# Performance work log

Measured on AMD Instinct MI355X. Metric: run time of the kernel, lower is better.

Reference implementation:

```python
import jax, jax.numpy as jnp
import numpy as np

# ---- module hyperparams (match init_kwargs) ----
REGIONS_DIMS = [0, 1, 2, 4, 9, 16]
ALL_DIM = sum(REGIONS_DIMS)          # 32
NUM_REGIONS = len(REGIONS_DIMS)      # 6
FIELD_NUM = 32
VOCAB = 200000
BATCH = 8192
TEMPERATURE = 1.0
EPS = 1e-5                            # torch BatchNorm1d default eps


def _build_region_mask():
    """Replicates init_variables(): row 0 is all-zero (drop-feature region),
    rows 1..R-1 are disjoint consecutive segments of sizes REGIONS_DIMS[1:]."""
    mask = np.zeros((NUM_REGIONS, ALL_DIM), dtype=np.float32)
    dims_pre_sum = [0] + [sum(REGIONS_DIMS[1:i]) for i in range(2, NUM_REGIONS)]
    for r, (pre, dim) in enumerate(zip(dims_pre_sum, REGIONS_DIMS[1:]), start=1):
        mask[r, pre:pre + dim] = 1.0
    return jnp.asarray(mask)


def setup_inputs() -> dict:
    key = jax.random.key(0)
    k_ids, k_emb, k_w = jax.random.split(key, 3)
    input_ids = jax.random.randint(k_ids, (BATCH, FIELD_NUM), 0, VOCAB, dtype=jnp.int64)
    # torch.nn.init.uniform_(a=-0.05, b=0.05)
    emb_table = jax.random.uniform(k_emb, (VOCAB, ALL_DIM), dtype=jnp.float32,
                                   minval=-0.05, maxval=0.05)
    # xavier_uniform on [F, R, 1]: bound = sqrt(6/(R+1))
    bound = float(np.sqrt(6.0 / (NUM_REGIONS + 1)))
    field_region_weights = jax.random.uniform(
        k_w, (FIELD_NUM, NUM_REGIONS, 1), dtype=jnp.float32, minval=-bound, maxval=bound)
    return {
        "input_ids": input_ids,
        "emb_table": emb_table,
        "field_region_weights": field_region_weights,
        "region_mask": _build_region_mask(),
    }


def reference(input_ids, emb_table, field_region_weights, region_mask):
    # Embedding gather: [B, F, D]
    emb = emb_table[input_ids]
    # BatchNorm1d(field_num, affine=False), training mode: per-field stats over (batch, D),
    # biased variance (torch normalizes with biased var).
    mean = jnp.mean(emb, axis=(0, 2), keepdims=True)
    var = jnp.var(emb, axis=(0, 2), keepdims=True)
    x = (emb - mean) * jax.lax.rsqrt(var + EPS)
    # softmax over regions: [F, R]
    w = jax.nn.softmax(field_region_weights[..., 0] / TEMPERATURE, axis=1)
    # sum_r w[f,r] * mask[r,d] -> per-(field, dim) scale; equivalent to the original's
    # broadcast-to-[B,F,R,D], multiply, and sum over R, without the big intermediate.
    coef = jnp.einsum('fr,rd->fd', w, region_mask)
    return x * coef[None, :, :]
```

## Files before the change

### kernel.cpp

```cpp
#include <hip/hip_runtime.h>
#include <math.h>

#define BATCH    8192
#define FIELDS   32
#define DIM      32
#define NREG     6
#define EPS      1e-5f
#define NBLKA    4096
#define PBASE    64


__global__ __launch_bounds__(256) void irazor_stats_kernel(
        const int*   __restrict__ ids,
        const float* __restrict__ table,
        float*       __restrict__ ws) {
    const int t   = threadIdx.x;
    const int blk = blockIdx.x;
    const int f   = t >> 3;
    const int vec = t & 7;

    float s = 0.f, sq = 0.f;
    #pragma unroll
    for (int i = 0; i < 2; ++i) {
        const int id = ids[(blk * 2 + i) * FIELDS + f];
        const float4 v = *reinterpret_cast<const float4*>(
            table + (size_t)id * DIM + vec * 4);
        s  += v.x + v.y + v.z + v.w;
        sq += v.x * v.x + v.y * v.y + v.z * v.z + v.w * v.w;
    }

    #pragma unroll
    for (int off = 1; off < 8; off <<= 1) {
        s  += __shfl_xor(s, off);
        sq += __shfl_xor(sq, off);
    }
    if (vec == 0) {
        ws[PBASE + f * NBLKA + blk]        = s;
        ws[PBASE + (32 + f) * NBLKA + blk] = sq;
    }
}

__global__ __launch_bounds__(256) void irazor_reduce_kernel(float* __restrict__ ws) {
    const int slot = blockIdx.x;
    const int t    = threadIdx.x;
    const float* __restrict__ p = ws + PBASE + (size_t)slot * NBLKA;
    float acc = 0.f;
    #pragma unroll
    for (int i = 0; i < NBLKA / 256; ++i) acc += p[i * 256 + t];
    #pragma unroll
    for (int off = 1; off < 64; off <<= 1) acc += __shfl_xor(acc, off);
    __shared__ float l[4];
    if ((t & 63) == 0) l[t >> 6] = acc;
    __syncthreads();
    if (t == 0) ws[slot] = l[0] + l[1] + l[2] + l[3];
}

__global__ __launch_bounds__(256) void irazor_out_kernel(
        const int*   __restrict__ ids,
        const float* __restrict__ table,
        const float* __restrict__ frw,
        const float* __restrict__ mask,
        const float* __restrict__ ws,
        float*       __restrict__ out) {
    const int t   = threadIdx.x;
    const int blk = blockIdx.x;

    __shared__ float scoef[FIELDS][DIM];
    {
        const int f2 = t & 31;
        const int q  = t >> 5;
        float w[NREG]; float m = -1e30f;
        #pragma unroll
        for (int r = 0; r < NREG; ++r) { w[r] = frw[f2 * NREG + r]; m = fmaxf(m, w[r]); }
        float ssum = 0.f;
        #pragma unroll
        for (int r = 0; r < NREG; ++r) { w[r] = __expf(w[r] - m); ssum += w[r]; }
        const float inv = 1.f / ssum;
        #pragma unroll
        for (int dd = 0; dd < 4; ++dd) {
            const int d = q * 4 + dd;
            float c = 0.f;
            #pragma unroll
            for (int r = 0; r < NREG; ++r) c += w[r] * mask[r * DIM + d];
            scoef[f2][d] = c * inv;
        }
    }
    __syncthreads();

    const int f   = t >> 3;
    const int vec = t & 7;
    const float invN = 1.f / (float)(BATCH * DIM);
    const float mean = ws[f] * invN;
    const float var  = ws[32 + f] * invN - mean * mean;
    const float istd = rsqrtf(var + EPS);
    const float4 c = *reinterpret_cast<const float4*>(&scoef[f][vec * 4]);

    float4* __restrict__ out4 = reinterpret_cast<float4*>(out);
    #pragma unroll
    for (int i = 0; i < 2; ++i) {
        const int id = ids[(blk * 2 + i) * FIELDS + f];
        const float4 v = *reinterpret_cast<const float4*>(
            table + (size_t)id * DIM + vec * 4);
        float4 o;
        o.x = (v.x - mean) * istd * c.x;
        o.y = (v.y - mean) * istd * c.y;
        o.z = (v.z - mean) * istd * c.z;
        o.w = (v.w - mean) * istd * c.w;
        out4[(size_t)blk * 512 + (size_t)i * 256 + t] = o;
    }
}

extern "C" void kernel_launch(void* const* d_in, const int* in_sizes, int n_in,
                              void* d_out, int out_size, void* d_ws, size_t ws_size,
                              hipStream_t stream) {
    const int*   ids   = (const int*)d_in[0];
    const float* table = (const float*)d_in[1];
    const float* frw   = (const float*)d_in[2];
    const float* mask  = (const float*)d_in[3];
    float*       out   = (float*)d_out;
    float*       ws    = (float*)d_ws;

    irazor_stats_kernel<<<NBLKA, 256, 0, stream>>>(ids, table, ws);
    irazor_reduce_kernel<<<64, 256, 0, stream>>>(ws);
    irazor_out_kernel<<<NBLKA, 256, 0, stream>>>(ids, table, frw, mask, ws, out);
}
```

Baseline: 100.1 us.

## Stage gathered embeddings in output buffer and apply precomputed scale/bias in place

The stats kernel now writes each gathered embedding row into the output buffer while accumulating sums. A finalize kernel reduces the partial sums per field and folds mean, inverse std and softmax region coefficients into per-(field,dim) scale and bias. The apply kernel then rewrites the output in place with one FMA, instead of re-gathering random table rows. This replaces a second random gather with a sequential read plus an extra full-size write.

```diff
diff --git a/kernel.cpp b/kernel.cpp
--- a/kernel.cpp
+++ b/kernel.cpp
@@ -8,23 +8,28 @@
 #define EPS      1e-5f
 #define NBLKA    4096
 #define PBASE    64
+#define SCALE_F  (PBASE + 64 * NBLKA)
+#define BIAS_F   (SCALE_F + FIELDS * DIM)
 
 
-__global__ __launch_bounds__(256) void irazor_stats_kernel(
+__global__ __launch_bounds__(256) void irazor_stage_stats_kernel(
         const int*   __restrict__ ids,
         const float* __restrict__ table,
-        float*       __restrict__ ws) {
+        float*       __restrict__ ws,
+        float*       __restrict__ out) {
     const int t   = threadIdx.x;
     const int blk = blockIdx.x;
     const int f   = t >> 3;
     const int vec = t & 7;
 
+    float4* __restrict__ out4 = reinterpret_cast<float4*>(out);
     float s = 0.f, sq = 0.f;
     #pragma unroll
     for (int i = 0; i < 2; ++i) {
         const int id = ids[(blk * 2 + i) * FIELDS + f];
         const float4 v = *reinterpret_cast<const float4*>(
             table + (size_t)id * DIM + vec * 4);
+        out4[(size_t)blk * 512 + (size_t)i * 256 + t] = v;
         s  += v.x + v.y + v.z + v.w;
         sq += v.x * v.x + v.y * v.y + v.z * v.z + v.w * v.w;
     }
@@ -40,73 +45,78 @@
     }
 }
 
-__global__ __launch_bounds__(256) void irazor_reduce_kernel(float* __restrict__ ws) {
-    const int slot = blockIdx.x;
-    const int t    = threadIdx.x;
-    const float* __restrict__ p = ws + PBASE + (size_t)slot * NBLKA;
-    float acc = 0.f;
+__global__ __launch_bounds__(256) void irazor_finalize_kernel(
+        const float* __restrict__ frw,
+        const float* __restrict__ mask,
+        float*       __restrict__ ws) {
+    const int fld = blockIdx.x;
+    const int t   = threadIdx.x;
+
+    const float* __restrict__ ps = ws + PBASE + (size_t)fld * NBLKA;
+    const float* __restrict__ pq = ws + PBASE + (size_t)(32 + fld) * NBLKA;
+    float a = 0.f, b = 0.f;
     #pragma unroll
-    for (int i = 0; i < NBLKA / 256; ++i) acc += p[i * 256 + t];
+    for (int i = 0; i < NBLKA / 256; ++i) {
+        a += ps[i * 256 + t];
+        b += pq[i * 256 + t];
+    }
     #pragma unroll
-    for (int off = 1; off < 64; off <<= 1) acc += __shfl_xor(acc, off);
-    __shared__ float l[4];
-    if ((t & 63) == 0) l[t >> 6] = acc;
+    for (int off = 1; off < 64; off <<= 1) {
+        a += __shfl_xor(a, off);
+        b += __shfl_xor(b, off);
+    }
+    __shared__ float ls[4], lq[4];
+    const int wave = t >> 6;
+    if ((t & 63) == 0) { ls[wave] = a; lq[wave] = b; }
     __syncthreads();
-    if (t == 0) ws[slot] = l[0] + l[1] + l[2] + l[3];
+    const float S  = ls[0] + ls[1] + ls[2] + ls[3];
+    const float SQ = lq[0] + lq[1] + lq[2] + lq[3];
+
+    if (t < DIM) {
+        const float invN = 1.f / (float)(BATCH * DIM);
+        const float mean = S * invN;
+        const float var  = SQ * invN - mean * mean;
+        const float istd = rsqrtf(var + EPS);
+
+        float w[NREG]; float m = -1e30f;
+        #pragma unroll
+        for (int r = 0; r < NREG; ++r) { w[r] = frw[fld * NREG + r]; m = fmaxf(m, w[r]); }
+        float ssum = 0.f;
+        #pragma unroll
+        for (int r = 0; r < NREG; ++r) { w[r] = __expf(w[r] - m); ssum += w[r]; }
+        float c = 0.f;
+        #pragma unroll
+        for (int r = 0; r < NREG; ++r) c += w[r] * mask[r * DIM + t];
+        c /= ssum;
+
+        const float sc = istd * c;
+        ws[SCALE_F + fld * DIM + t] = sc;
+        ws[BIAS_F  + fld * DIM + t] = -mean * sc;
+    }
 }
 
-__global__ __launch_bounds__(256) void irazor_out_kernel(
-        const int*   __restrict__ ids,
-        const float* __restrict__ table,
-        const float* __restrict__ frw,
-        const float* __restrict__ mask,
+__global__ __launch_bounds__(256) void irazor_apply_kernel(
         const float* __restrict__ ws,
         float*       __restrict__ out) {
     const int t   = threadIdx.x;
     const int blk = blockIdx.x;
-
-    __shared__ float scoef[FIELDS][DIM];
-    {
-        const int f2 = t & 31;
-        const int q  = t >> 5;
-        float w[NREG]; float m = -1e30f;
-        #pragma unroll
-        for (int r = 0; r < NREG; ++r) { w[r] = frw[f2 * NREG + r]; m = fmaxf(m, w[r]); }
-        float ssum = 0.f;
-        #pragma unroll
-        for (int r = 0; r < NREG; ++r) { w[r] = __expf(w[r] - m); ssum += w[r]; }
-        const float inv = 1.f / ssum;
-        #pragma unroll
-        for (int dd = 0; dd < 4; ++dd) {
-            const int d = q * 4 + dd;
-            float c = 0.f;
-            #pragma unroll
-            for (int r = 0; r < NREG; ++r) c += w[r] * mask[r * DIM + d];
-            scoef[f2][d] = c * inv;
-        }
-    }
-    __syncthreads();
-
     const int f   = t >> 3;
     const int vec = t & 7;
-    const float invN = 1.f / (float)(BATCH * DIM);
-    const float mean = ws[f] * invN;
-    const float var  = ws[32 + f] * invN - mean * mean;
-    const float istd = rsqrtf(var + EPS);
-    const float4 c = *reinterpret_cast<const float4*>(&scoef[f][vec * 4]);
+
+    const float4 sc = *reinterpret_cast<const float4*>(ws + SCALE_F + f * DIM + vec * 4);
+    const float4 bi = *reinterpret_cast<const float4*>(ws + BIAS_F  + f * DIM + vec * 4);
 
     float4* __restrict__ out4 = reinterpret_cast<float4*>(out);
     #pragma unroll
     for (int i = 0; i < 2; ++i) {
-        const int id = ids[(blk * 2 + i) * FIELDS + f];
-        const float4 v = *reinterpret_cast<const float4*>(
-            table + (size_t)id * DIM + vec * 4);
+        const size_t idx = (size_t)blk * 512 + (size_t)i * 256 + t;
+        float4 v = out4[idx];
         float4 o;
-        o.x = (v.x - mean) * istd * c.x;
-        o.y = (v.y - mean) * istd * c.y;
-        o.z = (v.z - mean) * istd * c.z;
-        o.w = (v.w - mean) * istd * c.w;
-        out4[(size_t)blk * 512 + (size_t)i * 256 + t] = o;
+        o.x = fmaf(v.x, sc.x, bi.x);
+        o.y = fmaf(v.y, sc.y, bi.y);
+        o.z = fmaf(v.z, sc.z, bi.z);
+        o.w = fmaf(v.w, sc.w, bi.w);
+        out4[idx] = o;
     }
 }
 
@@ -120,7 +130,7 @@
     float*       out   = (float*)d_out;
     float*       ws    = (float*)d_ws;
 
-    irazor_stats_kernel<<<NBLKA, 256, 0, stream>>>(ids, table, ws);
-    irazor_reduce_kernel<<<64, 256, 0, stream>>>(ws);
-    irazor_out_kernel<<<NBLKA, 256, 0, stream>>>(ids, table, frw, mask, ws, out);
+    irazor_stage_stats_kernel<<<NBLKA, 256, 0, stream>>>(ids, table, ws, out);
+    irazor_finalize_kernel<<<FIELDS, 256, 0, stream>>>(frw, mask, ws);
+    irazor_apply_kernel<<<NBLKA, 256, 0, stream>>>(ws, out);
 }
```

After: 105.6 us. +5.4%, slower.
